# Performance work log

Hardware: AMD Instinct MI355X
Metric: run time of the kernel (lower is better)

## Reference

```python
import jax, jax.numpy as jnp
import numpy as np

B, T, C, H = 2, 2048, 1024, 16
HS = C // H  # head size = 64


def _rope_cos_sin(t, hs):
    # theta_i = 1/10000^(2(i-1)/hs) for i in [1, hs/2]
    pos = jnp.arange(t, dtype=jnp.float32)[:, None]          # [T,1]
    i = jnp.arange(1, hs // 2 + 1, dtype=jnp.float32)[None]  # [1,hs/2]
    theta = 1.0 / 10000.0 ** (2.0 * (i - 1.0) / hs)
    ang = pos * theta                                        # [T,hs/2]
    return jnp.cos(ang), jnp.sin(ang)


def _apply_rope(u, cos, sin):
    # u: [B,H,T,HS]; complex multiply on consecutive pairs
    u2 = u.reshape(*u.shape[:-1], HS // 2, 2)
    x0, x1 = u2[..., 0], u2[..., 1]
    c = cos[None, None]  # [1,1,T,hs/2]
    s = sin[None, None]
    r0 = x0 * c - x1 * s
    r1 = x0 * s + x1 * c
    return jnp.stack([r0, r1], axis=-1).reshape(u.shape)


def setup_inputs() -> dict:
    key = jax.random.key(0)
    ks = jax.random.split(key, 5)
    return {
        "x": jax.random.normal(ks[0], (B, T, C), dtype=jnp.float32),
        "W_qkv": jax.random.normal(ks[1], (C, 3 * C), dtype=jnp.float32) * 0.02,
        "b_qkv": jax.random.normal(ks[2], (3 * C,), dtype=jnp.float32) * 0.02,
        "W_proj": jax.random.normal(ks[3], (C, C), dtype=jnp.float32) * 0.02,
        "b_proj": jax.random.normal(ks[4], (C,), dtype=jnp.float32) * 0.02,
    }


def reference(x, W_qkv, b_qkv, W_proj, b_proj):
    b, t, c = x.shape
    qkv = x @ W_qkv + b_qkv                                   # [B,T,3C]
    qkv = qkv.reshape(b, t, H, 3 * HS).transpose(0, 2, 1, 3)  # [B,H,T,3*HS]
    q, k, v = jnp.split(qkv, 3, axis=-1)                      # each [B,H,T,HS]

    cos, sin = _rope_cos_sin(t, HS)
    q = _apply_rope(q, cos, sin)
    k = _apply_rope(k, cos, sin)

    att = jnp.einsum("bhqd,bhkd->bhqk", q, k) / jnp.sqrt(jnp.float32(HS))
    causal = jnp.tril(jnp.ones((t, t), dtype=bool))[None, None]
    att = jnp.where(causal, att, jnp.float32(-1e9))
    att = jax.nn.softmax(att, axis=-1)
    y = jnp.einsum("bhqk,bhkd->bhqd", att, v)                 # [B,H,T,HS]
    y = y.transpose(0, 2, 1, 3).reshape(b, t, c)
    return y @ W_proj + b_proj
```

## Files before the change

kernel.cpp:

```cpp
#include <hip/hip_runtime.h>

typedef unsigned short u16;
typedef unsigned int u32;
typedef __bf16 bf16x8 __attribute__((ext_vector_type(8)));
typedef float f32x4 __attribute__((ext_vector_type(4)));
typedef u16 u16x4 __attribute__((ext_vector_type(4)));
typedef u16 u16x8 __attribute__((ext_vector_type(8)));

__device__ __forceinline__ u16 f2bf(float f) {
  u32 u = __builtin_bit_cast(u32, f);
  u += 0x7fffu + ((u >> 16) & 1u);
  return (u16)(u >> 16);
}

__device__ __forceinline__ u32 pk2(float a, float b) {
  u32 ua = __builtin_bit_cast(u32, a) + 0x8000u;
  u32 ub = __builtin_bit_cast(u32, b) + 0x8000u;
  return __builtin_amdgcn_perm(ub, ua, 0x07060302);
}

__device__ __forceinline__ void gld16(const void* g, void* l) {
  __builtin_amdgcn_global_load_lds(
      (const __attribute__((address_space(1))) void*)g,
      (__attribute__((address_space(3))) void*)l, 16, 0, 0);
}

__global__ __launch_bounds__(256) void k_prep(
    const float* __restrict__ x, u16* __restrict__ xb,
    const float* __restrict__ Wqkv, u16* __restrict__ Wqkvt,
    const float* __restrict__ Wproj, u16* __restrict__ Wpt,
    float2* __restrict__ rope) {
  __shared__ float tile[32][33];
  const int tid = threadIdx.x;
  int bx = blockIdx.x;
  if (bx < 4096) {
    int i = (bx * 256 + tid) * 4;
    float4 v = *(const float4*)(x + i);
    u16x4 o = { f2bf(v.x), f2bf(v.y), f2bf(v.z), f2bf(v.w) };
    *(u16x4*)(xb + i) = o;
    return;
  }
  bx -= 4096;
  const float* src; u16* dst; int R, Cc, bxx, byy;
  if (bx < 3072) {
    src = Wqkv; dst = Wqkvt; R = 1024; Cc = 3072; bxx = bx % 96; byy = bx / 96;
  } else if (bx < 4096) {
    int b = bx - 3072;
    src = Wproj; dst = Wpt; R = 1024; Cc = 1024; bxx = b % 32; byy = b / 32;
  } else {
    int i = (bx - 4096) * 256 + tid;
    int t = i >> 5, d = i & 31;
    float theta = expf(-(float)d * 0.28782313662425575f);
    float ang = (float)t * theta;
    rope[i] = make_float2(cosf(ang), sinf(ang));
    return;
  }
  int xx = tid & 31, yy = tid >> 5;
  int c0 = bxx * 32, r0 = byy * 32;
  for (int i = 0; i < 4; ++i)
    tile[yy + 8 * i][xx] = src[(size_t)(r0 + yy + 8 * i) * Cc + c0 + xx];
  __syncthreads();
  for (int i = 0; i < 4; ++i)
    dst[(size_t)(c0 + yy + 8 * i) * R + r0 + xx] = f2bf(tile[xx][yy + 8 * i]);
}

__global__ __launch_bounds__(256, 4) void k_qkv(
    const u16* __restrict__ Xb,
    const u16* __restrict__ Wt,
    const float* __restrict__ bias,
    const float2* __restrict__ rope,
    u16* __restrict__ Qg,
    u16* __restrict__ Kg,
    u16* __restrict__ Vt) {
  __shared__ alignas(16) u16 smem[18432];
  u16* As = smem;
  u16* Bs = smem + 8192;
  const int tid = threadIdx.x;
  const int lane = tid & 63, w = tid >> 6;
  const int quad = lane >> 4, l15 = lane & 15;
  const int m0 = blockIdx.y * 128, n0 = blockIdx.x * 128;
  const int wm = (w & 1) * 64, wn = (w >> 1) * 64;
  const int srow = lane >> 3, sj = lane & 7;
  const int sw = (sj ^ srow) * 8;
  const f32x4 vzero = {0.f, 0.f, 0.f, 0.f};

  f32x4 acc[4][4];
  for (int i = 0; i < 4; ++i)
    for (int j = 0; j < 4; ++j) acc[i][j] = vzero;

  for (int kt = 0; kt < 1024; kt += 64) {
    __syncthreads();
    for (int i = 0; i < 4; ++i) {
      int row = w * 32 + i * 8;
      gld16(Xb + (size_t)(m0 + row + srow) * 1024 + kt + sw, &As[row * 64]);
      gld16(Wt + (size_t)(n0 + row + srow) * 1024 + kt + sw, &Bs[row * 64]);
    }
    __syncthreads();
    for (int ks = 0; ks < 2; ++ks) {
      const int cc = ((ks * 4 + quad) ^ (l15 & 7)) * 8;
      bf16x8 a[4], b[4];
      for (int mt = 0; mt < 4; ++mt)
        a[mt] = *(const bf16x8*)&As[(wm + mt * 16 + l15) * 64 + cc];
      for (int nt = 0; nt < 4; ++nt)
        b[nt] = *(const bf16x8*)&Bs[(wn + nt * 16 + l15) * 64 + cc];
      for (int nt = 0; nt < 4; ++nt)
        for (int mt = 0; mt < 4; ++mt)
          acc[nt][mt] = __builtin_amdgcn_mfma_f32_16x16x32_bf16(
              b[nt], a[mt], acc[nt][mt], 0, 0, 0);
    }
  }
  __syncthreads();

  const int half = w >> 1;
  const int nh = n0 + half * 64;
  const int region = (nh % 192) >> 6;
  u16* Eh = smem + half * 9216;
  if (region < 2) {
    for (int nt = 0; nt < 4; ++nt) {
      float4 bv4 = *(const float4*)&bias[nh + nt * 16 + quad * 4];
      for (int mt = 0; mt < 4; ++mt) {
        int m_l = wm + mt * 16 + l15;
        int t = (m0 + m_l) & 2047;
        float4 cs = *(const float4*)&rope[t * 32 + nt * 8 + quad * 2];
        float v0 = acc[nt][mt][0] + bv4.x;
        float v1 = acc[nt][mt][1] + bv4.y;
        float v2 = acc[nt][mt][2] + bv4.z;
        float v3 = acc[nt][mt][3] + bv4.w;
        float r0 = fmaf(-v1, cs.y, v0 * cs.x);
        float r1 = fmaf( v0, cs.y, v1 * cs.x);
        float r2 = fmaf(-v3, cs.w, v2 * cs.z);
        float r3 = fmaf( v2, cs.w, v3 * cs.z);
        uint2 pv; pv.x = pk2(r0, r1); pv.y = pk2(r2, r3);
        *(uint2*)&Eh[m_l * 72 + nt * 16 + quad * 4] = pv;
      }
    }
  } else {
    for (int nt = 0; nt < 4; ++nt) {
      float4 bv4 = *(const float4*)&bias[nh + nt * 16 + quad * 4];
      for (int mt = 0; mt < 4; ++mt) {
        int m_l = wm + mt * 16 + l15;
        int cb = nt * 16 + quad * 4;
        Eh[(cb + 0) * 136 + m_l] = f2bf(acc[nt][mt][0] + bv4.x);
        Eh[(cb + 1) * 136 + m_l] = f2bf(acc[nt][mt][1] + bv4.y);
        Eh[(cb + 2) * 136 + m_l] = f2bf(acc[nt][mt][2] + bv4.z);
        Eh[(cb + 3) * 136 + m_l] = f2bf(acc[nt][mt][3] + bv4.w);
      }
    }
  }
  __syncthreads();

  const int bb = m0 >> 11, t0 = m0 & 2047;
  for (int hf = 0; hf < 2; ++hf) {
    const int nhf = n0 + hf * 64;
    const int hh = nhf / 192;
    const int reg = (nhf % 192) >> 6;
    const u16* Ef = smem + hf * 9216;
    if (reg < 2) {
      u16* dst = (reg == 0 ? Qg : Kg) +
                 ((size_t)(bb * 16 + hh) * 2048 + t0) * 64;
      int chunk = tid & 7, row0 = tid >> 3;
      for (int p = 0; p < 4; ++p) {
        int row = row0 + p * 32;
        u16x8 val = *(const u16x8*)&Ef[row * 72 + chunk * 8];
        *(u16x8*)(dst + (size_t)row * 64 + chunk * 8) = val;
      }
    } else {
      u16* dstv = Vt + (size_t)(bb * 16 + hh) * 64 * 2048 + t0;
      int mch = tid & 15, c0r = tid >> 4;
      for (int p = 0; p < 4; ++p) {
        int c = c0r + p * 16;
        u16x8 val = *(const u16x8*)&Ef[c * 136 + mch * 8];
        *(u16x8*)(dstv + (size_t)c * 2048 + mch * 8) = val;
      }
    }
  }
}

__global__ __launch_bounds__(256, 4) void k_attn(
    const u16* __restrict__ Qg, const u16* __restrict__ Kg,
    const u16* __restrict__ Vt, u16* __restrict__ Og) {
  __shared__ alignas(16) u16 Ks[2][64 * 64];
  __shared__ alignas(16) u16 Vs[2][64 * 64];
  __shared__ alignas(16) u16 Ps[64 * 72];
  const int tid = threadIdx.x, lane = tid & 63, w = tid >> 6;
  const int quad = lane >> 4, l15 = lane & 15;
  const int id = blockIdx.x;
  const int xr = id & 7, j = id >> 3;
  const int bx = j & 15;
  const int bh = (j >> 4) * 8 + xr;
  const u16* Qh = Qg + (size_t)bh * 2048 * 64;
  const u16* Kh = Kg + (size_t)bh * 2048 * 64;
  const u16* Vh = Vt + (size_t)bh * 64 * 2048;
  const f32x4 vzero = {0.f, 0.f, 0.f, 0.f};
  const float SCL = 0.125f * 1.4426950408889634f;
  const int myrow = w * 16;
  const int bb = bh >> 4, h = bh & 15;

  const int r8 = lane >> 3, j8 = lane & 7;
  const int sw_c = (j8 ^ r8) * 8;

  for (int i = 0; i < 2; ++i) {
    int row = w * 16 + i * 8;
    gld16(Kh + (size_t)(row + r8) * 64 + sw_c, &Ks[0][row * 64]);
    gld16(Vh + (size_t)(row + r8) * 2048 + sw_c, &Vs[0][row * 64]);
  }

  int buf = 0;
  const int tiles[2] = {bx, 31 - bx};
  for (int ti = 0; ti < 2; ++ti) {
    const int qt = tiles[ti];
    const int q0 = qt * 64;
    bf16x8 aq[2];
    {
      const u16* qp = Qh + (size_t)(q0 + myrow + l15) * 64 + quad * 8;
      aq[0] = *(const bf16x8*)(qp);
      aq[1] = *(const bf16x8*)(qp + 32);
    }
    float lsum = 0.f;
    f32x4 O[4];
    for (int nt = 0; nt < 4; ++nt) O[nt] = vzero;

    const int nk = qt + 1;
    for (int kb = 0; kb < nk; ++kb) {
      const int k0 = kb * 64;
      __syncthreads();
      int nxt = (kb + 1 < nk) ? (k0 + 64) : (ti == 0 ? 0 : -1);
      if (nxt >= 0) {
        for (int i = 0; i < 2; ++i) {
          int row = w * 16 + i * 8;
          gld16(Kh + (size_t)(nxt + row + r8) * 64 + sw_c, &Ks[buf ^ 1][row * 64]);
          gld16(Vh + (size_t)(row + r8) * 2048 + nxt + sw_c, &Vs[buf ^ 1][row * 64]);
        }
      }

      f32x4 st[4];
      for (int nt = 0; nt < 4; ++nt) st[nt] = vzero;
      for (int ks = 0; ks < 2; ++ks) {
        bf16x8 ak[4];
        for (int nt = 0; nt < 4; ++nt)
          ak[nt] = *(const bf16x8*)&Ks[buf][(nt * 16 + l15) * 64 +
                                           ((ks * 4 + quad) ^ (l15 & 7)) * 8];
        for (int nt = 0; nt < 4; ++nt)
          st[nt] = __builtin_amdgcn_mfma_f32_16x16x32_bf16(ak[nt], aq[ks], st[nt], 0, 0, 0);
      }

      if (kb < qt) {
        for (int nt = 0; nt < 4; ++nt) {
          float p0 = __builtin_amdgcn_exp2f(st[nt][0] * SCL);
          float p1 = __builtin_amdgcn_exp2f(st[nt][1] * SCL);
          float p2 = __builtin_amdgcn_exp2f(st[nt][2] * SCL);
          float p3 = __builtin_amdgcn_exp2f(st[nt][3] * SCL);
          lsum += (p0 + p1) + (p2 + p3);
          uint2 pv; pv.x = pk2(p0, p1); pv.y = pk2(p2, p3);
          *(uint2*)&Ps[(myrow + l15) * 72 + nt * 16 + quad * 4] = pv;
        }
      } else {
        const int tq = q0 + myrow + l15;
        const int kbase = k0 + quad * 4;
        for (int nt = 0; nt < 4; ++nt) {
          float p[4];
          for (int r = 0; r < 4; ++r) {
            float pv = __builtin_amdgcn_exp2f(st[nt][r] * SCL);
            p[r] = (kbase + nt * 16 + r <= tq) ? pv : 0.f;
            lsum += p[r];
          }
          uint2 pv; pv.x = pk2(p[0], p[1]); pv.y = pk2(p[2], p[3]);
          *(uint2*)&Ps[(myrow + l15) * 72 + nt * 16 + quad * 4] = pv;
        }
      }

      for (int ks = 0; ks < 2; ++ks) {
        bf16x8 a = *(const bf16x8*)&Ps[(myrow + l15) * 72 + ks * 32 + quad * 8];
        bf16x8 bv[4];
        for (int nt = 0; nt < 4; ++nt)
          bv[nt] = *(const bf16x8*)&Vs[buf][(nt * 16 + l15) * 64 +
                                           ((ks * 4 + quad) ^ (l15 & 7)) * 8];
        for (int nt = 0; nt < 4; ++nt)
          O[nt] = __builtin_amdgcn_mfma_f32_16x16x32_bf16(a, bv[nt], O[nt], 0, 0, 0);
      }
      buf ^= 1;
    }

    float ls = lsum;
    ls += __shfl_xor(ls, 16, 64);
    ls += __shfl_xor(ls, 32, 64);
    float inv[4];
    for (int r = 0; r < 4; ++r)
      inv[r] = 1.0f / __shfl(ls, quad * 4 + r, 16);

    for (int nt = 0; nt < 4; ++nt)
      for (int r = 0; r < 4; ++r)
        Ps[(myrow + quad * 4 + r) * 72 + nt * 16 + l15] = f2bf(O[nt][r] * inv[r]);
    __syncthreads();
    u16* dst = Og + ((size_t)bb * 2048 + q0) * 1024 + h * 64;
    int chunk = tid & 7, row0 = tid >> 3;
    for (int p = 0; p < 2; ++p) {
      int row = row0 + p * 32;
      u16x8 val = *(const u16x8*)&Ps[row * 72 + chunk * 8];
      *(u16x8*)(dst + (size_t)row * 1024 + chunk * 8) = val;
    }
  }
}

__global__ __launch_bounds__(256, 4) void k_proj(
    const u16* __restrict__ Ag,
    const u16* __restrict__ Wt,
    const float* __restrict__ bias,
    float* __restrict__ out) {
  __shared__ alignas(16) u16 As[64 * 64];
  __shared__ alignas(16) u16 Bs[128 * 64];
  const int tid = threadIdx.x;
  const int lane = tid & 63, w = tid >> 6;
  const int quad = lane >> 4, l15 = lane & 15;
  const int m0 = blockIdx.y * 64, n0 = blockIdx.x * 128;
  const int wm = (w & 1) * 32, wn = (w >> 1) * 64;
  const int srow = lane >> 3, sj = lane & 7;
  const int sw = (sj ^ srow) * 8;
  const f32x4 vzero = {0.f, 0.f, 0.f, 0.f};

  f32x4 acc[2][4];
  for (int i = 0; i < 2; ++i)
    for (int j = 0; j < 4; ++j) acc[i][j] = vzero;

  for (int kt = 0; kt < 1024; kt += 64) {
    __syncthreads();
    for (int i = 0; i < 2; ++i) {
      int row = w * 16 + i * 8;
      gld16(Ag + (size_t)(m0 + row + srow) * 1024 + kt + sw, &As[row * 64]);
    }
    for (int i = 0; i < 4; ++i) {
      int row = w * 32 + i * 8;
      gld16(Wt + (size_t)(n0 + row + srow) * 1024 + kt + sw, &Bs[row * 64]);
    }
    __syncthreads();
    for (int ks = 0; ks < 2; ++ks) {
      const int cc = ((ks * 4 + quad) ^ (l15 & 7)) * 8;
      bf16x8 a[2], b[4];
      for (int mt = 0; mt < 2; ++mt)
        a[mt] = *(const bf16x8*)&As[(wm + mt * 16 + l15) * 64 + cc];
      for (int nt = 0; nt < 4; ++nt)
        b[nt] = *(const bf16x8*)&Bs[(wn + nt * 16 + l15) * 64 + cc];
      for (int mt = 0; mt < 2; ++mt)
        for (int nt = 0; nt < 4; ++nt)
          acc[mt][nt] = __builtin_amdgcn_mfma_f32_16x16x32_bf16(
              a[mt], b[nt], acc[mt][nt], 0, 0, 0);
    }
  }

  for (int nt = 0; nt < 4; ++nt) {
    int n = n0 + wn + nt * 16 + l15;
    float bv = bias[n];
    for (int mt = 0; mt < 2; ++mt)
      for (int r = 0; r < 4; ++r) {
        int m = m0 + wm + mt * 16 + quad * 4 + r;
        out[(size_t)m * 1024 + n] = acc[mt][nt][r] + bv;
      }
  }
}

extern "C" void kernel_launch(void* const* d_in, const int* in_sizes, int n_in,
                              void* d_out, int out_size, void* d_ws, size_t ws_size,
                              hipStream_t stream) {
  (void)in_sizes; (void)n_in; (void)out_size; (void)ws_size;
  const float* x     = (const float*)d_in[0];
  const float* Wqkv  = (const float*)d_in[1];
  const float* bqkv  = (const float*)d_in[2];
  const float* Wproj = (const float*)d_in[3];
  const float* bproj = (const float*)d_in[4];
  float* out = (float*)d_out;

  char* ws = (char*)d_ws;
  size_t off = 0;
  u16* Xb    = (u16*)(ws + off); off += (size_t)4096 * 1024 * 2;
  u16* Wqkvt = (u16*)(ws + off); off += (size_t)3072 * 1024 * 2;
  u16* Wpt   = (u16*)(ws + off); off += (size_t)1024 * 1024 * 2;
  u16* Qg    = (u16*)(ws + off); off += (size_t)2 * 16 * 2048 * 64 * 2;
  u16* Kg    = (u16*)(ws + off); off += (size_t)2 * 16 * 2048 * 64 * 2;
  u16* Vt    = (u16*)(ws + off); off += (size_t)2 * 16 * 64 * 2048 * 2;
  u16* Att   = (u16*)(ws + off); off += (size_t)4096 * 1024 * 2;
  float2* rope = (float2*)(ws + off); off += (size_t)2048 * 32 * sizeof(float2);

  k_prep<<<8448, 256, 0, stream>>>(x, Xb, Wqkv, Wqkvt, Wproj, Wpt, rope);
  k_qkv<<<dim3(24, 32), 256, 0, stream>>>(Xb, Wqkvt, bqkv, rope, Qg, Kg, Vt);
  k_attn<<<512, 256, 0, stream>>>(Qg, Kg, Vt, Att);
  k_proj<<<dim3(8, 64), 256, 0, stream>>>(Att, Wpt, bproj, out);
}
```

Measured before the change: 171.0 us.

## Split attention into one query tile per block and fold softmax scale into Q

The attention kernel now launches one block per query tile (1024 blocks) instead of pairing tile bx with tile 31-bx in a single block. Tiles are mapped heavy-first with a per-head rotation to balance causal work. The softmax scale (1/8·log2e) is folded into Q during the QKV epilogue, which removes a multiply before each exp2. The P tile is stored unpadded with an XOR swizzle instead of a 72-element row pitch, which cuts LDS use. The cost is reloading the first K/V tile in every block and more scheduling variance across blocks. Q is also rounded to bf16 after scaling, which slightly changes numerics.

```diff
diff --git a/kernel.cpp b/kernel.cpp
--- a/kernel.cpp
+++ b/kernel.cpp
@@ -116,6 +116,7 @@
   const int region = (nh % 192) >> 6;
   u16* Eh = smem + half * 9216;
   if (region < 2) {
+    const float qsc = (region == 0) ? 0.18033688011112042f : 1.0f;
     for (int nt = 0; nt < 4; ++nt) {
       float4 bv4 = *(const float4*)&bias[nh + nt * 16 + quad * 4];
       for (int mt = 0; mt < 4; ++mt) {
@@ -126,10 +127,10 @@
         float v1 = acc[nt][mt][1] + bv4.y;
         float v2 = acc[nt][mt][2] + bv4.z;
         float v3 = acc[nt][mt][3] + bv4.w;
-        float r0 = fmaf(-v1, cs.y, v0 * cs.x);
-        float r1 = fmaf( v0, cs.y, v1 * cs.x);
-        float r2 = fmaf(-v3, cs.w, v2 * cs.z);
-        float r3 = fmaf( v2, cs.w, v3 * cs.z);
+        float r0 = fmaf(-v1, cs.y, v0 * cs.x) * qsc;
+        float r1 = fmaf( v0, cs.y, v1 * cs.x) * qsc;
+        float r2 = fmaf(-v3, cs.w, v2 * cs.z) * qsc;
+        float r3 = fmaf( v2, cs.w, v3 * cs.z) * qsc;
         uint2 pv; pv.x = pk2(r0, r1); pv.y = pk2(r2, r3);
         *(uint2*)&Eh[m_l * 72 + nt * 16 + quad * 4] = pv;
       }
@@ -181,23 +182,24 @@
     const u16* __restrict__ Vt, u16* __restrict__ Og) {
   __shared__ alignas(16) u16 Ks[2][64 * 64];
   __shared__ alignas(16) u16 Vs[2][64 * 64];
-  __shared__ alignas(16) u16 Ps[64 * 72];
+  __shared__ alignas(16) u16 Ps[64 * 64];
   const int tid = threadIdx.x, lane = tid & 63, w = tid >> 6;
   const int quad = lane >> 4, l15 = lane & 15;
   const int id = blockIdx.x;
   const int xr = id & 7, j = id >> 3;
-  const int bx = j & 15;
-  const int bh = (j >> 4) * 8 + xr;
+  const int bh = (j >> 5) * 8 + xr;
+  const int x32 = (j + 7 * (j >> 5)) & 31;
+  const int qt = (x32 & 1) ? (x32 >> 1) : (31 - (x32 >> 1));
   const u16* Qh = Qg + (size_t)bh * 2048 * 64;
   const u16* Kh = Kg + (size_t)bh * 2048 * 64;
   const u16* Vh = Vt + (size_t)bh * 64 * 2048;
   const f32x4 vzero = {0.f, 0.f, 0.f, 0.f};
-  const float SCL = 0.125f * 1.4426950408889634f;
   const int myrow = w * 16;
   const int bb = bh >> 4, h = bh & 15;
 
   const int r8 = lane >> 3, j8 = lane & 7;
   const int sw_c = (j8 ^ r8) * 8;
+  const int psw = (l15 & 7) << 1;
 
   for (int i = 0; i < 2; ++i) {
     int row = w * 16 + i * 8;
@@ -205,100 +207,102 @@
     gld16(Vh + (size_t)(row + r8) * 2048 + sw_c, &Vs[0][row * 64]);
   }
 
+  const int q0 = qt * 64;
+  bf16x8 aq[2];
+  {
+    const u16* qp = Qh + (size_t)(q0 + myrow + l15) * 64 + quad * 8;
+    aq[0] = *(const bf16x8*)(qp);
+    aq[1] = *(const bf16x8*)(qp + 32);
+  }
+  float lsum = 0.f;
+  f32x4 O[4];
+  for (int nt = 0; nt < 4; ++nt) O[nt] = vzero;
+
   int buf = 0;
-  const int tiles[2] = {bx, 31 - bx};
-  for (int ti = 0; ti < 2; ++ti) {
-    const int qt = tiles[ti];
-    const int q0 = qt * 64;
-    bf16x8 aq[2];
-    {
-      const u16* qp = Qh + (size_t)(q0 + myrow + l15) * 64 + quad * 8;
-      aq[0] = *(const bf16x8*)(qp);
-      aq[1] = *(const bf16x8*)(qp + 32);
-    }
-    float lsum = 0.f;
-    f32x4 O[4];
-    for (int nt = 0; nt < 4; ++nt) O[nt] = vzero;
-
-    const int nk = qt + 1;
-    for (int kb = 0; kb < nk; ++kb) {
-      const int k0 = kb * 64;
-      __syncthreads();
-      int nxt = (kb + 1 < nk) ? (k0 + 64) : (ti == 0 ? 0 : -1);
-      if (nxt >= 0) {
-        for (int i = 0; i < 2; ++i) {
-          int row = w * 16 + i * 8;
-          gld16(Kh + (size_t)(nxt + row + r8) * 64 + sw_c, &Ks[buf ^ 1][row * 64]);
-          gld16(Vh + (size_t)(row + r8) * 2048 + nxt + sw_c, &Vs[buf ^ 1][row * 64]);
+  const int nk = qt + 1;
+  for (int kb = 0; kb < nk; ++kb) {
+    const int k0 = kb * 64;
+    __syncthreads();
+    if (kb + 1 < nk) {
+      const int nxt = k0 + 64;
+      for (int i = 0; i < 2; ++i) {
+        int row = w * 16 + i * 8;
+        gld16(Kh + (size_t)(nxt + row + r8) * 64 + sw_c, &Ks[buf ^ 1][row * 64]);
+        gld16(Vh + (size_t)(row + r8) * 2048 + nxt + sw_c, &Vs[buf ^ 1][row * 64]);
+      }
+    }
+
+    f32x4 st[4];
+    for (int nt = 0; nt < 4; ++nt) st[nt] = vzero;
+    for (int ks = 0; ks < 2; ++ks) {
+      bf16x8 ak[4];
+      for (int nt = 0; nt < 4; ++nt)
+        ak[nt] = *(const bf16x8*)&Ks[buf][(nt * 16 + l15) * 64 +
+                                         ((ks * 4 + quad) ^ (l15 & 7)) * 8];
+      for (int nt = 0; nt < 4; ++nt)
+        st[nt] = __builtin_amdgcn_mfma_f32_16x16x32_bf16(ak[nt], aq[ks], st[nt], 0, 0, 0);
+    }
+
+    const int prow = myrow + l15;
+    if (kb < qt) {
+      for (int nt = 0; nt < 4; ++nt) {
+        float p0 = __builtin_amdgcn_exp2f(st[nt][0]);
+        float p1 = __builtin_amdgcn_exp2f(st[nt][1]);
+        float p2 = __builtin_amdgcn_exp2f(st[nt][2]);
+        float p3 = __builtin_amdgcn_exp2f(st[nt][3]);
+        lsum += (p0 + p1) + (p2 + p3);
+        uint2 pv; pv.x = pk2(p0, p1); pv.y = pk2(p2, p3);
+        *(uint2*)&Ps[prow * 64 + ((nt * 4 + quad) ^ psw) * 4] = pv;
+      }
+    } else {
+      const int tq = q0 + myrow + l15;
+      const int kbase = k0 + quad * 4;
+      for (int nt = 0; nt < 4; ++nt) {
+        float p[4];
+        for (int r = 0; r < 4; ++r) {
+          float pv = __builtin_amdgcn_exp2f(st[nt][r]);
+          p[r] = (kbase + nt * 16 + r <= tq) ? pv : 0.f;
+          lsum += p[r];
         }
-      }
-
-      f32x4 st[4];
-      for (int nt = 0; nt < 4; ++nt) st[nt] = vzero;
-      for (int ks = 0; ks < 2; ++ks) {
-        bf16x8 ak[4];
-        for (int nt = 0; nt < 4; ++nt)
-          ak[nt] = *(const bf16x8*)&Ks[buf][(nt * 16 + l15) * 64 +
-                                           ((ks * 4 + quad) ^ (l15 & 7)) * 8];
-        for (int nt = 0; nt < 4; ++nt)
-          st[nt] = __builtin_amdgcn_mfma_f32_16x16x32_bf16(ak[nt], aq[ks], st[nt], 0, 0, 0);
-      }
-
-      if (kb < qt) {
-        for (int nt = 0; nt < 4; ++nt) {
-          float p0 = __builtin_amdgcn_exp2f(st[nt][0] * SCL);
-          float p1 = __builtin_amdgcn_exp2f(st[nt][1] * SCL);
-          float p2 = __builtin_amdgcn_exp2f(st[nt][2] * SCL);
-          float p3 = __builtin_amdgcn_exp2f(st[nt][3] * SCL);
-          lsum += (p0 + p1) + (p2 + p3);
-          uint2 pv; pv.x = pk2(p0, p1); pv.y = pk2(p2, p3);
-          *(uint2*)&Ps[(myrow + l15) * 72 + nt * 16 + quad * 4] = pv;
-        }
-      } else {
-        const int tq = q0 + myrow + l15;
-        const int kbase = k0 + quad * 4;
-        for (int nt = 0; nt < 4; ++nt) {
-          float p[4];
-          for (int r = 0; r < 4; ++r) {
-            float pv = __builtin_amdgcn_exp2f(st[nt][r] * SCL);
-            p[r] = (kbase + nt * 16 + r <= tq) ? pv : 0.f;
-            lsum += p[r];
-          }
-          uint2 pv; pv.x = pk2(p[0], p[1]); pv.y = pk2(p[2], p[3]);
-          *(uint2*)&Ps[(myrow + l15) * 72 + nt * 16 + quad * 4] = pv;
-        }
-      }
-
-      for (int ks = 0; ks < 2; ++ks) {
-        bf16x8 a = *(const bf16x8*)&Ps[(myrow + l15) * 72 + ks * 32 + quad * 8];
-        bf16x8 bv[4];
-        for (int nt = 0; nt < 4; ++nt)
-          bv[nt] = *(const bf16x8*)&Vs[buf][(nt * 16 + l15) * 64 +
-                                           ((ks * 4 + quad) ^ (l15 & 7)) * 8];
-        for (int nt = 0; nt < 4; ++nt)
-          O[nt] = __builtin_amdgcn_mfma_f32_16x16x32_bf16(a, bv[nt], O[nt], 0, 0, 0);
-      }
-      buf ^= 1;
-    }
-
-    float ls = lsum;
-    ls += __shfl_xor(ls, 16, 64);
-    ls += __shfl_xor(ls, 32, 64);
-    float inv[4];
-    for (int r = 0; r < 4; ++r)
-      inv[r] = 1.0f / __shfl(ls, quad * 4 + r, 16);
-
-    for (int nt = 0; nt < 4; ++nt)
-      for (int r = 0; r < 4; ++r)
-        Ps[(myrow + quad * 4 + r) * 72 + nt * 16 + l15] = f2bf(O[nt][r] * inv[r]);
-    __syncthreads();
-    u16* dst = Og + ((size_t)bb * 2048 + q0) * 1024 + h * 64;
-    int chunk = tid & 7, row0 = tid >> 3;
-    for (int p = 0; p < 2; ++p) {
-      int row = row0 + p * 32;
-      u16x8 val = *(const u16x8*)&Ps[row * 72 + chunk * 8];
-      *(u16x8*)(dst + (size_t)row * 1024 + chunk * 8) = val;
-    }
+        uint2 pv; pv.x = pk2(p[0], p[1]); pv.y = pk2(p[2], p[3]);
+        *(uint2*)&Ps[prow * 64 + ((nt * 4 + quad) ^ psw) * 4] = pv;
+      }
+    }
+
+    for (int ks = 0; ks < 2; ++ks) {
+      bf16x8 a = *(const bf16x8*)&Ps[prow * 64 + ((ks * 8 + quad * 2) ^ psw) * 4];
+      bf16x8 bv[4];
+      for (int nt = 0; nt < 4; ++nt)
+        bv[nt] = *(const bf16x8*)&Vs[buf][(nt * 16 + l15) * 64 +
+                                         ((ks * 4 + quad) ^ (l15 & 7)) * 8];
+      for (int nt = 0; nt < 4; ++nt)
+        O[nt] = __builtin_amdgcn_mfma_f32_16x16x32_bf16(a, bv[nt], O[nt], 0, 0, 0);
+    }
+    buf ^= 1;
+  }
+
+  float ls = lsum;
+  ls += __shfl_xor(ls, 16, 64);
+  ls += __shfl_xor(ls, 32, 64);
+  float inv[4];
+  for (int r = 0; r < 4; ++r)
+    inv[r] = 1.0f / __shfl(ls, quad * 4 + r, 16);
+
+  for (int nt = 0; nt < 4; ++nt)
+    for (int r = 0; r < 4; ++r) {
+      int row = myrow + quad * 4 + r;
+      int col = nt * 16 + l15;
+      int up = (col >> 2) ^ ((row & 7) << 1);
+      Ps[row * 64 + up * 4 + (col & 3)] = f2bf(O[nt][r] * inv[r]);
+    }
+  __syncthreads();
+  u16* dst = Og + ((size_t)bb * 2048 + q0) * 1024 + h * 64;
+  int chunk = tid & 7, row0 = tid >> 3;
+  for (int p = 0; p < 2; ++p) {
+    int row = row0 + p * 32;
+    int up = (chunk * 2) ^ ((row & 7) << 1);
+    u16x8 val = *(const u16x8*)&Ps[row * 64 + up * 4];
+    *(u16x8*)(dst + (size_t)row * 1024 + chunk * 8) = val;
   }
 }
 
@@ -382,6 +386,6 @@
 
   k_prep<<<8448, 256, 0, stream>>>(x, Xb, Wqkv, Wqkvt, Wproj, Wpt, rope);
   k_qkv<<<dim3(24, 32), 256, 0, stream>>>(Xb, Wqkvt, bqkv, rope, Qg, Kg, Vt);
-  k_attn<<<512, 256, 0, stream>>>(Qg, Kg, Vt, Att);
+  k_attn<<<1024, 256, 0, stream>>>(Qg, Kg, Vt, Att);
   k_proj<<<dim3(8, 64), 256, 0, stream>>>(Att, Wpt, bproj, out);
 }
```

Result: slower. 175.7 us (+2.8%).
